# Kernel tuning notes

Measured on AMD Instinct MI355X. Metric: run time of the kernel, lower is better.

The kernel has to match this reference:

```python
import jax, jax.numpy as jnp
import numpy as np

V, E, H = 1024, 32, 64
D = 8                     # number of tree levels (root at depth 0)
PER = 149796              # nodes per non-root level
N = 1 + 7 * PER           # 1048573 total nodes


def setup_inputs() -> dict:
    rng = np.random.default_rng(0)
    sizes = [1] + [PER] * (D - 1)
    off = np.concatenate([[0], np.cumsum(sizes)])
    depth = np.repeat(np.arange(D), sizes).astype(np.int64)
    parent = np.zeros(N, dtype=np.int64)  # root points to itself (harmless: its h is 0 when read)
    for l in range(1, D):
        parent[off[l]:off[l + 1]] = rng.integers(off[l - 1], off[l], sizes[l])
    token_ids = rng.integers(0, V, N).astype(np.int64)

    key = jax.random.key(0)
    ks = jax.random.split(key, 7)
    s = 0.05
    return {
        "token_ids": jnp.asarray(token_ids),
        "parent": jnp.asarray(parent),
        "depth": jnp.asarray(depth),
        "max_depth": D - 1,
        "emb": jax.random.normal(ks[0], (V, E), jnp.float32) * s,
        "W_iou_w": jax.random.normal(ks[1], (3 * H, E), jnp.float32) * s,
        "W_iou_b": jax.random.normal(ks[2], (3 * H,), jnp.float32) * s,
        "U_iou_w": jax.random.normal(ks[3], (3 * H, H), jnp.float32) * s,
        "W_f_w": jax.random.normal(ks[4], (H, E), jnp.float32) * s,
        "W_f_b": jax.random.normal(ks[5], (H,), jnp.float32) * s,
        "U_f_w": jax.random.normal(ks[6], (H, H), jnp.float32) * s,
    }


def reference(token_ids, parent, depth, max_depth, emb,
              W_iou_w, W_iou_b, U_iou_w, W_f_w, W_f_b, U_f_w):
    n = token_ids.shape[0]
    hid = U_f_w.shape[0]
    x = emb[token_ids]                                 # [N, E]
    wiou_x = x @ W_iou_w.T + W_iou_b                   # [N, 3H] (input part, precomputed)
    wf_x = x @ W_f_w.T + W_f_b                         # [N, H]
    h = jnp.zeros((n, hid), x.dtype)
    c = jnp.zeros((n, hid), x.dtype)
    # level-synchronous bottom-up sweep (deepest level first); children of a
    # depth-d node are exactly at depth d+1, already finalized when d is processed
    for d in range(max_depth, -1, -1):
        h_sum = jax.ops.segment_sum(h, parent, num_segments=n)        # child-sum per parent
        f = jax.nn.sigmoid(wf_x[parent] + h @ U_f_w.T)                # forget gate per child edge
        fc = jax.ops.segment_sum(f * c, parent, num_segments=n)      # sum_k f_k * c_k per parent
        iou = wiou_x + h_sum @ U_iou_w.T
        i, o, u = jnp.split(iou, 3, axis=-1)
        c_new = jax.nn.sigmoid(i) * jnp.tanh(u) + fc
        h_new = jax.nn.sigmoid(o) * jnp.tanh(c_new)
        m = (depth == d)[:, None]
        h = jnp.where(m, h_new, h)
        c = jnp.where(m, c_new, c)
    return h[0]  # root hidden state, matching TreeLSTMEncoder.forward
```

## Files before the change

kernel.cpp:

```cpp
#include <hip/hip_runtime.h>
#include <hip/hip_fp16.h>
#include <string.h>

#define PER  149796
#define NN   1048573
#define HDIM 64
#define EDIM 32
#define NIOU 192

typedef _Float16 f16;
typedef _Float16 f16x8 __attribute__((ext_vector_type(8)));
typedef _Float16 f16x2 __attribute__((ext_vector_type(2)));
typedef float    f32x4 __attribute__((ext_vector_type(4)));

__device__ __forceinline__ float sigf(float x){ return 1.0f/(1.0f+__expf(-x)); }
__device__ __forceinline__ float tanh_f(float x){
  float ax = fabsf(x);
  float e  = __expf(-2.0f*ax);
  float t  = (1.0f - e)/(1.0f + e);
  return x < 0.0f ? -t : t;
}

__device__ __forceinline__ void atomAddH2(f16x2* p, f16 a, f16 b){
#if defined(__HIP_DEVICE_COMPILE__)
  typedef _Float16 h2 __attribute__((ext_vector_type(2)));
  h2 v; v[0]=a; v[1]=b;
  (void)__builtin_amdgcn_global_atomic_fadd_v2f16(
      (__attribute__((address_space(1))) h2*)p, v);
#else
  (void)p; (void)a; (void)b;
#endif
}

__global__ __launch_bounds__(256) void tablepack_kernel(
    const float* __restrict__ emb, const float* __restrict__ Wiou, const float* __restrict__ biou,
    const float* __restrict__ Wf, const float* __restrict__ bf,
    const float* __restrict__ Uf, const float* __restrict__ Uiou,
    float* __restrict__ embWiou, float* __restrict__ embWf,
    f16* __restrict__ Bfp, f16* __restrict__ Biop)
{
  if (blockIdx.x < 1024){
    int v = blockIdx.x;
    int m = threadIdx.x;
    const float* x = emb + (size_t)v*EDIM;
    if (m < NIOU){
      float a = biou[m];
      #pragma unroll
      for (int e=0;e<EDIM;e++) a += Wiou[m*EDIM+e]*x[e];
      embWiou[(size_t)v*NIOU + m] = a;
    } else {
      int mm = m - NIOU;
      float a = bf[mm];
      #pragma unroll
      for (int e=0;e<EDIM;e++) a += Wf[mm*EDIM+e]*x[e];
      embWf[(size_t)v*HDIM + mm] = a;
    }
  } else {
    for (int i = threadIdx.x; i < 2*4*64*8; i += 256){
      int j = i & 7, L = (i>>3)&63, st = i>>9;
      int t = st & 3, s = st >> 2;
      int k = s*32 + (L>>4)*8 + j;
      int n = t*16 + (L&15);
      Bfp[i] = (f16)Uf[n*HDIM + k];
    }
    for (int i = threadIdx.x; i < 2*12*64*8; i += 256){
      int j = i & 7, L = (i>>3)&63, st = i>>9;
      int t = st % 12, s = st / 12;
      int k = s*32 + (L>>4)*8 + j;
      int n = t*16 + (L&15);
      Biop[i] = (f16)Uiou[n*HDIM + k];
    }
  }
}

__global__ __launch_bounds__(64,4) void level_kernel(
    const int* __restrict__ tok, const int* __restrict__ parent,
    const float* __restrict__ embWiou, const float* __restrict__ embWf,
    const f16* __restrict__ Biopack, const f16* __restrict__ Ufpack,
    const f16x2* __restrict__ accIn, f16x2* __restrict__ accOut,
    int poff, int ppoff, int mode)
{
  __shared__ f16 Ah[16*72];
  __shared__ f16 FAf[16*68];
  int lane = threadIdx.x;
  int j0   = blockIdx.x*16;
  int q = lane>>4, c16 = lane&15;

  if (mode != 0){
    #pragma unroll
    for (int i=0;i<16;i++){
      int j = j0 + i; if (j > PER-1) j = PER-1;
      f16x2 v = accIn[(size_t)j*HDIM + lane];
      Ah[i*72 + lane]  = v.x;
      FAf[i*68 + lane] = v.y;
    }
  } else {
    #pragma unroll
    for (int i=0;i<16;i++){
      Ah[i*72 + lane]  = (f16)0.f;
      FAf[i*68 + lane] = (f16)0.f;
    }
  }
  __syncthreads();
  f16x8 A0 = *(const f16x8*)(Ah + c16*72 + q*8);
  f16x8 A1 = *(const f16x8*)(Ah + c16*72 + 32 + q*8);

  const f16x8* Bp = (const f16x8*)Biopack;
  f32x4 acc[12];
  #pragma unroll
  for (int nt=0;nt<12;nt++) acc[nt] = (f32x4){0.f,0.f,0.f,0.f};
  #pragma unroll
  for (int nt=0;nt<12;nt++){
    f16x8 B0 = Bp[nt*64 + lane];
    f16x8 B1 = Bp[(12+nt)*64 + lane];
    acc[nt] = __builtin_amdgcn_mfma_f32_16x16x32_f16(A0, B0, acc[nt], 0,0,0);
    acc[nt] = __builtin_amdgcn_mfma_f32_16x16x32_f16(A1, B1, acc[nt], 0,0,0);
  }
  float cc[4][4];
  f16   hh[4][4];
  int   prow_[4]; int wt_[4]; bool ok_[4];
  #pragma unroll
  for (int r=0;r<4;r++){
    int j = j0 + q*4 + r;
    bool ok = j < PER;
    int jl = ok ? j : PER-1;
    int g = poff + jl;
    int tk = tok[g];
    const float* tr = embWiou + (size_t)tk*NIOU;
    ok_[r] = ok;
    if (mode != 2){
      int pg = parent[g];
      prow_[r] = pg - ppoff;
      wt_[r]   = tok[pg];
    } else {
      prow_[r] = jl;
      wt_[r]   = tok[0];
    }
    int prow = q*4 + r;
    #pragma unroll
    for (int nt=0;nt<4;nt++){
      int col = nt*16 + c16;
      float ai = acc[nt][r]   + tr[col];
      float ao = acc[nt+4][r] + tr[64+col];
      float au = acc[nt+8][r] + tr[128+col];
      float fav = (float)FAf[prow*68 + col];
      float c = sigf(ai)*tanh_f(au) + fav;
      float h = sigf(ao)*tanh_f(c);
      cc[r][nt] = c;
      hh[r][nt] = (f16)h;
    }
  }
  __syncthreads();
  #pragma unroll
  for (int r=0;r<4;r++)
    #pragma unroll
    for (int nt=0;nt<4;nt++)
      Ah[(q*4+r)*72 + nt*16 + c16] = hh[r][nt];
  __syncthreads();
  f16x8 H0 = *(const f16x8*)(Ah + c16*72 + q*8);
  f16x8 H1 = *(const f16x8*)(Ah + c16*72 + 32 + q*8);
  const f16x8* Up = (const f16x8*)Ufpack;
  f32x4 g4[4];
  #pragma unroll
  for (int nt=0;nt<4;nt++) g4[nt] = (f32x4){0.f,0.f,0.f,0.f};
  #pragma unroll
  for (int nt=0;nt<4;nt++){
    f16x8 B0 = Up[nt*64 + lane];
    f16x8 B1 = Up[(4+nt)*64 + lane];
    g4[nt] = __builtin_amdgcn_mfma_f32_16x16x32_f16(H0, B0, g4[nt], 0,0,0);
    g4[nt] = __builtin_amdgcn_mfma_f32_16x16x32_f16(H1, B1, g4[nt], 0,0,0);
  }
  #pragma unroll
  for (int r=0;r<4;r++){
    if (!ok_[r]) continue;
    const float* wr = embWf + (size_t)wt_[r]*HDIM;
    size_t rb = (size_t)prow_[r]*HDIM;
    #pragma unroll
    for (int nt=0;nt<4;nt++){
      int col = nt*16 + c16;
      float v = sigf(g4[nt][r] + wr[col]) * cc[r][nt];
      if (mode == 2){
        f16x2 o; o.x = hh[r][nt]; o.y = (f16)v;
        accOut[rb + col] = o;
      } else {
        atomAddH2(&accOut[rb + col], hh[r][nt], (f16)v);
      }
    }
  }
}

__global__ __launch_bounds__(256) void rootred_kernel(
    const f16x2* __restrict__ HFin, float* __restrict__ rootacc)
{
  int t = blockIdx.x*blockDim.x + threadIdx.x;
  int m = t & 63;
  int j0 = t >> 6;
  int jstep = (gridDim.x*blockDim.x) >> 6;
  float af=0.f, ah=0.f;
  for (int j=j0; j<PER; j+=jstep){
    f16x2 v = HFin[(size_t)j*HDIM + m];
    ah += (float)v.x;
    af += (float)v.y;
  }
  __shared__ float red[256];
  red[threadIdx.x]=af; __syncthreads();
  if (threadIdx.x < 64) atomicAdd(&rootacc[m],    red[m]+red[64+m]+red[128+m]+red[192+m]);
  __syncthreads();
  red[threadIdx.x]=ah; __syncthreads();
  if (threadIdx.x < 64) atomicAdd(&rootacc[64+m], red[m]+red[64+m]+red[128+m]+red[192+m]);
}

__global__ void rootnode_kernel(
    const int* __restrict__ tok, const float* __restrict__ emb,
    const float* __restrict__ Wiou, const float* __restrict__ biou, const float* __restrict__ Uiou,
    const float* __restrict__ rootacc, float* __restrict__ out)
{
  int m = threadIdx.x;
  if (m >= HDIM) return;
  int t = tok[0];
  float ai=biou[m], ao=biou[HDIM+m], au=biou[2*HDIM+m];
  for (int e=0;e<EDIM;e++){
    float xe = emb[(size_t)t*EDIM+e];
    ai += Wiou[(size_t)m*EDIM+e]*xe;
    ao += Wiou[(size_t)(HDIM+m)*EDIM+e]*xe;
    au += Wiou[(size_t)(2*HDIM+m)*EDIM+e]*xe;
  }
  for (int k=0;k<HDIM;k++){
    float hv = rootacc[64+k];
    ai += Uiou[(size_t)m*HDIM+k]*hv;
    ao += Uiou[(size_t)(HDIM+m)*HDIM+k]*hv;
    au += Uiou[(size_t)(2*HDIM+m)*HDIM+k]*hv;
  }
  float c = sigf(ai)*tanh_f(au) + rootacc[m];
  out[m] = sigf(ao)*tanh_f(c);
}

static inline char* alignup(char* p){
  uintptr_t u = (uintptr_t)p;
  u = (u + 255) & ~(uintptr_t)255;
  return (char*)u;
}

extern "C" void kernel_launch(void* const* d_in, const int* in_sizes, int n_in,
                              void* d_out, int out_size, void* d_ws, size_t ws_size,
                              hipStream_t stream)
{
  const int*   tok    = (const int*)d_in[0];
  const int*   parent = (const int*)d_in[1];
  const float* emb    = (const float*)d_in[4];
  const float* Wiou   = (const float*)d_in[5];
  const float* biou   = (const float*)d_in[6];
  const float* Uiou   = (const float*)d_in[7];
  const float* Wf     = (const float*)d_in[8];
  const float* bf     = (const float*)d_in[9];
  const float* Uf     = (const float*)d_in[10];
  float* out = (float*)d_out;

  char* w = (char*)d_ws;
  size_t BUF = (size_t)PER*HDIM*sizeof(f16x2);
  f16x2* bufA    = (f16x2*)w;  w = alignup(w + BUF);
  f16x2* bufB    = (f16x2*)w;  w = alignup(w + BUF);
  float* embWiou = (float*)w;  w = alignup(w + 1024*NIOU*sizeof(float));
  float* embWf   = (float*)w;  w = alignup(w + 1024*HDIM*sizeof(float));
  float* rootacc = (float*)w;  w = alignup(w + 128*sizeof(float));
  f16*   Ufpack  = (f16*)w;    w = alignup(w + 2*4*64*8*sizeof(f16));
  f16*   Biopack = (f16*)w;    w = alignup(w + 2*12*64*8*sizeof(f16));

  const int NB = (PER + 15)/16;

  (void)hipMemsetAsync(rootacc, 0, 128*sizeof(float), stream);
  tablepack_kernel<<<1025, 256, 0, stream>>>(emb, Wiou, biou, Wf, bf, Uf, Uiou,
                                             embWiou, embWf, Ufpack, Biopack);

  f16x2* accIn  = nullptr;
  f16x2* accOut = bufA;
  (void)hipMemsetAsync(bufA, 0, BUF, stream);
  level_kernel<<<NB, 64, 0, stream>>>(tok, parent, embWiou, embWf, Biopack, Ufpack,
                                      nullptr, bufA, 1 + 6*PER, 1 + 5*PER, 0);
  accIn = bufA; accOut = bufB;
  for (int d=6; d>=2; --d){
    (void)hipMemsetAsync(accOut, 0, BUF, stream);
    level_kernel<<<NB, 64, 0, stream>>>(tok, parent, embWiou, embWf, Biopack, Ufpack,
                                        accIn, accOut, 1 + (d-1)*PER, 1 + (d-2)*PER, 1);
    f16x2* t2 = accIn; accIn = accOut; accOut = t2;
  }
  level_kernel<<<NB, 64, 0, stream>>>(tok, parent, embWiou, embWf, Biopack, Ufpack,
                                      accIn, accOut, 1, 0, 2);

  rootred_kernel<<<256, 256, 0, stream>>>(accOut, rootacc);
  rootnode_kernel<<<1, 64, 0, stream>>>(tok, emb, Wiou, biou, Uiou, rootacc, out);
}
```

Measured before the change: 550.6 us.

## Fuse input projections into level MFMA and zero consumed buffers in-kernel

Drops the precomputed per-token fp32 embWiou/embWf tables. The level kernel now gathers fp16 embeddings and runs the W_iou and W_f projections as an extra K=32 MFMA slice, adding the biases directly. Each block now holds four waves (256 threads) with per-wave shared tiles and no block barriers, and the leaf level skips the zero h-sum MFMAs. The per-level memsets are replaced by zeroing accIn inside the kernel after it is read. This trades large fp32 table gathers and memset launches for extra MFMA work and a reduced-precision input projection.

```diff
diff --git a/kernel.cpp b/kernel.cpp
--- a/kernel.cpp
+++ b/kernel.cpp
@@ -33,77 +33,83 @@
 }
 
 __global__ __launch_bounds__(256) void tablepack_kernel(
-    const float* __restrict__ emb, const float* __restrict__ Wiou, const float* __restrict__ biou,
-    const float* __restrict__ Wf, const float* __restrict__ bf,
+    const float* __restrict__ emb, const float* __restrict__ Wiou,
+    const float* __restrict__ Wf,
     const float* __restrict__ Uf, const float* __restrict__ Uiou,
-    float* __restrict__ embWiou, float* __restrict__ embWf,
+    f16* __restrict__ emb16,
     f16* __restrict__ Bfp, f16* __restrict__ Biop)
 {
   if (blockIdx.x < 1024){
     int v = blockIdx.x;
     int m = threadIdx.x;
-    const float* x = emb + (size_t)v*EDIM;
-    if (m < NIOU){
-      float a = biou[m];
-      #pragma unroll
-      for (int e=0;e<EDIM;e++) a += Wiou[m*EDIM+e]*x[e];
-      embWiou[(size_t)v*NIOU + m] = a;
-    } else {
-      int mm = m - NIOU;
-      float a = bf[mm];
-      #pragma unroll
-      for (int e=0;e<EDIM;e++) a += Wf[mm*EDIM+e]*x[e];
-      embWf[(size_t)v*HDIM + mm] = a;
-    }
+    if (m < EDIM) emb16[(size_t)v*EDIM + m] = (f16)emb[(size_t)v*EDIM + m];
   } else {
-    for (int i = threadIdx.x; i < 2*4*64*8; i += 256){
+    for (int i = threadIdx.x; i < 3*4*64*8; i += 256){
       int j = i & 7, L = (i>>3)&63, st = i>>9;
       int t = st & 3, s = st >> 2;
-      int k = s*32 + (L>>4)*8 + j;
+      int kk = (L>>4)*8 + j;
       int n = t*16 + (L&15);
-      Bfp[i] = (f16)Uf[n*HDIM + k];
-    }
-    for (int i = threadIdx.x; i < 2*12*64*8; i += 256){
+      Bfp[i] = (s < 2) ? (f16)Uf[n*HDIM + s*32 + kk]
+                       : (f16)Wf[n*EDIM + kk];
+    }
+    for (int i = threadIdx.x; i < 3*12*64*8; i += 256){
       int j = i & 7, L = (i>>3)&63, st = i>>9;
       int t = st % 12, s = st / 12;
-      int k = s*32 + (L>>4)*8 + j;
+      int kk = (L>>4)*8 + j;
       int n = t*16 + (L&15);
-      Biop[i] = (f16)Uiou[n*HDIM + k];
-    }
-  }
-}
-
-__global__ __launch_bounds__(64,4) void level_kernel(
+      Biop[i] = (s < 2) ? (f16)Uiou[n*HDIM + s*32 + kk]
+                        : (f16)Wiou[n*EDIM + kk];
+    }
+  }
+}
+
+__global__ __launch_bounds__(256,7) void level_kernel(
     const int* __restrict__ tok, const int* __restrict__ parent,
-    const float* __restrict__ embWiou, const float* __restrict__ embWf,
+    const f16* __restrict__ emb16,
+    const float* __restrict__ biou, const float* __restrict__ bf,
     const f16* __restrict__ Biopack, const f16* __restrict__ Ufpack,
     const f16x2* __restrict__ accIn, f16x2* __restrict__ accOut,
-    int poff, int ppoff, int mode)
-{
-  __shared__ f16 Ah[16*72];
-  __shared__ f16 FAf[16*68];
-  int lane = threadIdx.x;
-  int j0   = blockIdx.x*16;
+    int poff, int ppoff, int mode, int zin)
+{
+  __shared__ f16 Ah[4][16*104];
+  __shared__ f16 FAf[4][16*68];
+  int lane = threadIdx.x & 63;
+  int w    = threadIdx.x >> 6;
+  int j0   = (blockIdx.x*4 + w)*16;
   int q = lane>>4, c16 = lane&15;
-
+  f16* AhW  = &Ah[w][0];
+  f16* FAfW = &FAf[w][0];
+
+  {
+    int i  = lane>>2, cb = lane&3;
+    int j  = j0 + i; if (j > PER-1) j = PER-1;
+    int tk = tok[poff + j];
+    f16x8 xv = *(const f16x8*)(emb16 + (size_t)tk*EDIM + cb*8);
+    *(f16x8*)(AhW + i*104 + 64 + cb*8) = xv;
+  }
   if (mode != 0){
     #pragma unroll
     for (int i=0;i<16;i++){
       int j = j0 + i; if (j > PER-1) j = PER-1;
       f16x2 v = accIn[(size_t)j*HDIM + lane];
-      Ah[i*72 + lane]  = v.x;
-      FAf[i*68 + lane] = v.y;
+      AhW[i*104 + lane]  = v.x;
+      FAfW[i*68 + lane] = v.y;
     }
   } else {
     #pragma unroll
+    for (int i=0;i<16;i++)
+      FAfW[i*68 + lane] = (f16)0.f;
+  }
+  f16x8 A2 = *(const f16x8*)(AhW + c16*104 + 64 + q*8);
+
+  if (mode != 0 && zin){
+    f16x2 z; z.x = (f16)0.f; z.y = (f16)0.f;
+    #pragma unroll
     for (int i=0;i<16;i++){
-      Ah[i*72 + lane]  = (f16)0.f;
-      FAf[i*68 + lane] = (f16)0.f;
-    }
-  }
-  __syncthreads();
-  f16x8 A0 = *(const f16x8*)(Ah + c16*72 + q*8);
-  f16x8 A1 = *(const f16x8*)(Ah + c16*72 + 32 + q*8);
+      int j = j0 + i;
+      if (j < PER) ((f16x2*)accIn)[(size_t)j*HDIM + lane] = z;
+    }
+  }
 
   const f16x8* Bp = (const f16x8*)Biopack;
   f32x4 acc[12];
@@ -111,54 +117,61 @@
   for (int nt=0;nt<12;nt++) acc[nt] = (f32x4){0.f,0.f,0.f,0.f};
   #pragma unroll
   for (int nt=0;nt<12;nt++){
-    f16x8 B0 = Bp[nt*64 + lane];
-    f16x8 B1 = Bp[(12+nt)*64 + lane];
-    acc[nt] = __builtin_amdgcn_mfma_f32_16x16x32_f16(A0, B0, acc[nt], 0,0,0);
-    acc[nt] = __builtin_amdgcn_mfma_f32_16x16x32_f16(A1, B1, acc[nt], 0,0,0);
+    f16x8 B2 = Bp[(24+nt)*64 + lane];
+    acc[nt] = __builtin_amdgcn_mfma_f32_16x16x32_f16(A2, B2, acc[nt], 0,0,0);
+  }
+  if (mode != 0){
+    f16x8 A0 = *(const f16x8*)(AhW + c16*104 + q*8);
+    f16x8 A1 = *(const f16x8*)(AhW + c16*104 + 32 + q*8);
+    #pragma unroll
+    for (int nt=0;nt<12;nt++){
+      f16x8 B0 = Bp[nt*64 + lane];
+      f16x8 B1 = Bp[(12+nt)*64 + lane];
+      acc[nt] = __builtin_amdgcn_mfma_f32_16x16x32_f16(A0, B0, acc[nt], 0,0,0);
+      acc[nt] = __builtin_amdgcn_mfma_f32_16x16x32_f16(A1, B1, acc[nt], 0,0,0);
+    }
   }
   float cc[4][4];
   f16   hh[4][4];
-  int   prow_[4]; int wt_[4]; bool ok_[4];
+  int   prow_[4]; bool ok_[4];
   #pragma unroll
   for (int r=0;r<4;r++){
     int j = j0 + q*4 + r;
     bool ok = j < PER;
     int jl = ok ? j : PER-1;
     int g = poff + jl;
-    int tk = tok[g];
-    const float* tr = embWiou + (size_t)tk*NIOU;
     ok_[r] = ok;
-    if (mode != 2){
-      int pg = parent[g];
-      prow_[r] = pg - ppoff;
-      wt_[r]   = tok[pg];
-    } else {
-      prow_[r] = jl;
-      wt_[r]   = tok[0];
-    }
+    prow_[r] = (mode != 2) ? (parent[g] - ppoff) : jl;
     int prow = q*4 + r;
     #pragma unroll
     for (int nt=0;nt<4;nt++){
       int col = nt*16 + c16;
-      float ai = acc[nt][r]   + tr[col];
-      float ao = acc[nt+4][r] + tr[64+col];
-      float au = acc[nt+8][r] + tr[128+col];
-      float fav = (float)FAf[prow*68 + col];
+      float ai = acc[nt][r]   + biou[col];
+      float ao = acc[nt+4][r] + biou[64+col];
+      float au = acc[nt+8][r] + biou[128+col];
+      float fav = (float)FAfW[prow*68 + col];
       float c = sigf(ai)*tanh_f(au) + fav;
       float h = sigf(ao)*tanh_f(c);
       cc[r][nt] = c;
       hh[r][nt] = (f16)h;
     }
   }
-  __syncthreads();
   #pragma unroll
   for (int r=0;r<4;r++)
     #pragma unroll
     for (int nt=0;nt<4;nt++)
-      Ah[(q*4+r)*72 + nt*16 + c16] = hh[r][nt];
-  __syncthreads();
-  f16x8 H0 = *(const f16x8*)(Ah + c16*72 + q*8);
-  f16x8 H1 = *(const f16x8*)(Ah + c16*72 + 32 + q*8);
+      AhW[(q*4+r)*104 + nt*16 + c16] = hh[r][nt];
+  {
+    int i  = lane>>2, cb = lane&3;
+    int j  = j0 + i; if (j > PER-1) j = PER-1;
+    int pg = (mode != 2) ? parent[poff + j] : 0;
+    int ptk = tok[pg];
+    f16x8 pv = *(const f16x8*)(emb16 + (size_t)ptk*EDIM + cb*8);
+    *(f16x8*)(AhW + i*104 + 64 + cb*8) = pv;
+  }
+  f16x8 H0 = *(const f16x8*)(AhW + c16*104 + q*8);
+  f16x8 H1 = *(const f16x8*)(AhW + c16*104 + 32 + q*8);
+  f16x8 H2 = *(const f16x8*)(AhW + c16*104 + 64 + q*8);
   const f16x8* Up = (const f16x8*)Ufpack;
   f32x4 g4[4];
   #pragma unroll
@@ -167,18 +180,19 @@
   for (int nt=0;nt<4;nt++){
     f16x8 B0 = Up[nt*64 + lane];
     f16x8 B1 = Up[(4+nt)*64 + lane];
+    f16x8 B2 = Up[(8+nt)*64 + lane];
     g4[nt] = __builtin_amdgcn_mfma_f32_16x16x32_f16(H0, B0, g4[nt], 0,0,0);
     g4[nt] = __builtin_amdgcn_mfma_f32_16x16x32_f16(H1, B1, g4[nt], 0,0,0);
+    g4[nt] = __builtin_amdgcn_mfma_f32_16x16x32_f16(H2, B2, g4[nt], 0,0,0);
   }
   #pragma unroll
   for (int r=0;r<4;r++){
     if (!ok_[r]) continue;
-    const float* wr = embWf + (size_t)wt_[r]*HDIM;
     size_t rb = (size_t)prow_[r]*HDIM;
     #pragma unroll
     for (int nt=0;nt<4;nt++){
       int col = nt*16 + c16;
-      float v = sigf(g4[nt][r] + wr[col]) * cc[r][nt];
+      float v = sigf(g4[nt][r] + bf[col]) * cc[r][nt];
       if (mode == 2){
         f16x2 o; o.x = hh[r][nt]; o.y = (f16)v;
         accOut[rb + col] = o;
@@ -260,32 +274,32 @@
   size_t BUF = (size_t)PER*HDIM*sizeof(f16x2);
   f16x2* bufA    = (f16x2*)w;  w = alignup(w + BUF);
   f16x2* bufB    = (f16x2*)w;  w = alignup(w + BUF);
-  float* embWiou = (float*)w;  w = alignup(w + 1024*NIOU*sizeof(float));
-  float* embWf   = (float*)w;  w = alignup(w + 1024*HDIM*sizeof(float));
   float* rootacc = (float*)w;  w = alignup(w + 128*sizeof(float));
-  f16*   Ufpack  = (f16*)w;    w = alignup(w + 2*4*64*8*sizeof(f16));
-  f16*   Biopack = (f16*)w;    w = alignup(w + 2*12*64*8*sizeof(f16));
-
-  const int NB = (PER + 15)/16;
+  f16*   emb16   = (f16*)w;    w = alignup(w + 1024*EDIM*sizeof(f16));
+  f16*   Ufpack  = (f16*)w;    w = alignup(w + 3*4*64*8*sizeof(f16));
+  f16*   Biopack = (f16*)w;    w = alignup(w + 3*12*64*8*sizeof(f16));
+
+  const int NB = (PER + 63)/64;
 
   (void)hipMemsetAsync(rootacc, 0, 128*sizeof(float), stream);
-  tablepack_kernel<<<1025, 256, 0, stream>>>(emb, Wiou, biou, Wf, bf, Uf, Uiou,
-                                             embWiou, embWf, Ufpack, Biopack);
+  (void)hipMemsetAsync(bufA, 0, BUF, stream);
+  (void)hipMemsetAsync(bufB, 0, BUF, stream);
+  tablepack_kernel<<<1025, 256, 0, stream>>>(emb, Wiou, Wf, Uf, Uiou,
+                                             emb16, Ufpack, Biopack);
 
   f16x2* accIn  = nullptr;
   f16x2* accOut = bufA;
-  (void)hipMemsetAsync(bufA, 0, BUF, stream);
-  level_kernel<<<NB, 64, 0, stream>>>(tok, parent, embWiou, embWf, Biopack, Ufpack,
-                                      nullptr, bufA, 1 + 6*PER, 1 + 5*PER, 0);
+  level_kernel<<<NB, 256, 0, stream>>>(tok, parent, emb16, biou, bf, Biopack, Ufpack,
+                                       nullptr, bufA, 1 + 6*PER, 1 + 5*PER, 0, 0);
   accIn = bufA; accOut = bufB;
   for (int d=6; d>=2; --d){
-    (void)hipMemsetAsync(accOut, 0, BUF, stream);
-    level_kernel<<<NB, 64, 0, stream>>>(tok, parent, embWiou, embWf, Biopack, Ufpack,
-                                        accIn, accOut, 1 + (d-1)*PER, 1 + (d-2)*PER, 1);
+    level_kernel<<<NB, 256, 0, stream>>>(tok, parent, emb16, biou, bf, Biopack, Ufpack,
+                                         accIn, accOut, 1 + (d-1)*PER, 1 + (d-2)*PER, 1,
+                                         (d >= 3) ? 1 : 0);
     f16x2* t2 = accIn; accIn = accOut; accOut = t2;
   }
-  level_kernel<<<NB, 64, 0, stream>>>(tok, parent, embWiou, embWf, Biopack, Ufpack,
-                                      accIn, accOut, 1, 0, 2);
+  level_kernel<<<NB, 256, 0, stream>>>(tok, parent, emb16, biou, bf, Biopack, Ufpack,
+                                       accIn, accOut, 1, 0, 2, 0);
 
   rootred_kernel<<<256, 256, 0, stream>>>(accOut, rootacc);
   rootnode_kernel<<<1, 64, 0, stream>>>(tok, emb, Wiou, biou, Uiou, rootacc, out);
```

Measured after the change: 937.1 us. 1.7x slower.

## Pack IOU table as float4, use 4-wave blocks, fold buffer zeroing into kernel

Applied to the files above, without the earlier changes.

Repacks the per-token input-gate table so i/o/u for a column are fetched with one 16-byte load. Launches four 16-row tiles per 256-thread block with per-wave shared buffers instead of single-wave blocks. Replaces per-level hipMemsetAsync of the accumulation buffer with in-kernel zeroing of the consumed input buffer after it is read, removing separate memset passes. The in-kernel zeroing depends on buffer ping-pong parity, which risks leaving stale data in the final level's output buffer.

```diff
diff --git a/kernel.cpp b/kernel.cpp
--- a/kernel.cpp
+++ b/kernel.cpp
@@ -36,23 +36,29 @@
     const float* __restrict__ emb, const float* __restrict__ Wiou, const float* __restrict__ biou,
     const float* __restrict__ Wf, const float* __restrict__ bf,
     const float* __restrict__ Uf, const float* __restrict__ Uiou,
-    float* __restrict__ embWiou, float* __restrict__ embWf,
+    f32x4* __restrict__ packIOU, float* __restrict__ embWf,
     f16* __restrict__ Bfp, f16* __restrict__ Biop)
 {
   if (blockIdx.x < 1024){
     int v = blockIdx.x;
     int m = threadIdx.x;
     const float* x = emb + (size_t)v*EDIM;
-    if (m < NIOU){
-      float a = biou[m];
+    if (m < HDIM){
+      float a = biou[m], b = biou[HDIM+m], c = biou[2*HDIM+m];
       #pragma unroll
-      for (int e=0;e<EDIM;e++) a += Wiou[m*EDIM+e]*x[e];
-      embWiou[(size_t)v*NIOU + m] = a;
-    } else {
-      int mm = m - NIOU;
+      for (int e=0;e<EDIM;e++){
+        float xe = x[e];
+        a += Wiou[(size_t)m*EDIM+e]*xe;
+        b += Wiou[(size_t)(HDIM+m)*EDIM+e]*xe;
+        c += Wiou[(size_t)(2*HDIM+m)*EDIM+e]*xe;
+      }
+      f32x4 o; o.x=a; o.y=b; o.z=c; o.w=0.f;
+      packIOU[(size_t)v*HDIM + m] = o;
+    } else if (m < 2*HDIM){
+      int mm = m - HDIM;
       float a = bf[mm];
       #pragma unroll
-      for (int e=0;e<EDIM;e++) a += Wf[mm*EDIM+e]*x[e];
+      for (int e=0;e<EDIM;e++) a += Wf[(size_t)mm*EDIM+e]*x[e];
       embWf[(size_t)v*HDIM + mm] = a;
     }
   } else {
@@ -73,37 +79,49 @@
   }
 }
 
-__global__ __launch_bounds__(64,4) void level_kernel(
+__global__ __launch_bounds__(256,8) void level_kernel(
     const int* __restrict__ tok, const int* __restrict__ parent,
-    const float* __restrict__ embWiou, const float* __restrict__ embWf,
+    const f32x4* __restrict__ packIOU, const float* __restrict__ embWf,
     const f16* __restrict__ Biopack, const f16* __restrict__ Ufpack,
     const f16x2* __restrict__ accIn, f16x2* __restrict__ accOut,
-    int poff, int ppoff, int mode)
-{
-  __shared__ f16 Ah[16*72];
-  __shared__ f16 FAf[16*68];
-  int lane = threadIdx.x;
-  int j0   = blockIdx.x*16;
+    int poff, int ppoff, int mode, int zin)
+{
+  __shared__ f16 Ah[4][16*72];
+  __shared__ f16 FAf[4][16*68];
+  int lane = threadIdx.x & 63;
+  int w    = threadIdx.x >> 6;
+  int j0   = (blockIdx.x*4 + w)*16;
   int q = lane>>4, c16 = lane&15;
+  f16* AhW  = &Ah[w][0];
+  f16* FAfW = &FAf[w][0];
 
   if (mode != 0){
     #pragma unroll
     for (int i=0;i<16;i++){
       int j = j0 + i; if (j > PER-1) j = PER-1;
       f16x2 v = accIn[(size_t)j*HDIM + lane];
-      Ah[i*72 + lane]  = v.x;
-      FAf[i*68 + lane] = v.y;
+      AhW[i*72 + lane]  = v.x;
+      FAfW[i*68 + lane] = v.y;
     }
   } else {
     #pragma unroll
     for (int i=0;i<16;i++){
-      Ah[i*72 + lane]  = (f16)0.f;
-      FAf[i*68 + lane] = (f16)0.f;
+      AhW[i*72 + lane]  = (f16)0.f;
+      FAfW[i*68 + lane] = (f16)0.f;
     }
   }
   __syncthreads();
-  f16x8 A0 = *(const f16x8*)(Ah + c16*72 + q*8);
-  f16x8 A1 = *(const f16x8*)(Ah + c16*72 + 32 + q*8);
+  f16x8 A0 = *(const f16x8*)(AhW + c16*72 + q*8);
+  f16x8 A1 = *(const f16x8*)(AhW + c16*72 + 32 + q*8);
+
+  if (mode != 0 && zin){
+    f16x2 z; z.x = (f16)0.f; z.y = (f16)0.f;
+    #pragma unroll
+    for (int i=0;i<16;i++){
+      int j = j0 + i;
+      if (j < PER) ((f16x2*)accIn)[(size_t)j*HDIM + lane] = z;
+    }
+  }
 
   const f16x8* Bp = (const f16x8*)Biopack;
   f32x4 acc[12];
@@ -126,7 +144,7 @@
     int jl = ok ? j : PER-1;
     int g = poff + jl;
     int tk = tok[g];
-    const float* tr = embWiou + (size_t)tk*NIOU;
+    const f32x4* tr = packIOU + (size_t)tk*HDIM;
     ok_[r] = ok;
     if (mode != 2){
       int pg = parent[g];
@@ -140,10 +158,11 @@
     #pragma unroll
     for (int nt=0;nt<4;nt++){
       int col = nt*16 + c16;
-      float ai = acc[nt][r]   + tr[col];
-      float ao = acc[nt+4][r] + tr[64+col];
-      float au = acc[nt+8][r] + tr[128+col];
-      float fav = (float)FAf[prow*68 + col];
+      f32x4 wx = tr[col];
+      float ai = acc[nt][r]   + wx.x;
+      float ao = acc[nt+4][r] + wx.y;
+      float au = acc[nt+8][r] + wx.z;
+      float fav = (float)FAfW[prow*68 + col];
       float c = sigf(ai)*tanh_f(au) + fav;
       float h = sigf(ao)*tanh_f(c);
       cc[r][nt] = c;
@@ -155,10 +174,10 @@
   for (int r=0;r<4;r++)
     #pragma unroll
     for (int nt=0;nt<4;nt++)
-      Ah[(q*4+r)*72 + nt*16 + c16] = hh[r][nt];
+      AhW[(q*4+r)*72 + nt*16 + c16] = hh[r][nt];
   __syncthreads();
-  f16x8 H0 = *(const f16x8*)(Ah + c16*72 + q*8);
-  f16x8 H1 = *(const f16x8*)(Ah + c16*72 + 32 + q*8);
+  f16x8 H0 = *(const f16x8*)(AhW + c16*72 + q*8);
+  f16x8 H1 = *(const f16x8*)(AhW + c16*72 + 32 + q*8);
   const f16x8* Up = (const f16x8*)Ufpack;
   f32x4 g4[4];
   #pragma unroll
@@ -260,32 +279,33 @@
   size_t BUF = (size_t)PER*HDIM*sizeof(f16x2);
   f16x2* bufA    = (f16x2*)w;  w = alignup(w + BUF);
   f16x2* bufB    = (f16x2*)w;  w = alignup(w + BUF);
-  float* embWiou = (float*)w;  w = alignup(w + 1024*NIOU*sizeof(float));
+  f32x4* packIOU = (f32x4*)w;  w = alignup(w + (size_t)1024*HDIM*sizeof(f32x4));
   float* embWf   = (float*)w;  w = alignup(w + 1024*HDIM*sizeof(float));
   float* rootacc = (float*)w;  w = alignup(w + 128*sizeof(float));
   f16*   Ufpack  = (f16*)w;    w = alignup(w + 2*4*64*8*sizeof(f16));
   f16*   Biopack = (f16*)w;    w = alignup(w + 2*12*64*8*sizeof(f16));
 
-  const int NB = (PER + 15)/16;
+  const int NB = (PER + 63)/64;
 
   (void)hipMemsetAsync(rootacc, 0, 128*sizeof(float), stream);
+  (void)hipMemsetAsync(bufA, 0, BUF, stream);
+  (void)hipMemsetAsync(bufB, 0, BUF, stream);
   tablepack_kernel<<<1025, 256, 0, stream>>>(emb, Wiou, biou, Wf, bf, Uf, Uiou,
-                                             embWiou, embWf, Ufpack, Biopack);
+                                             packIOU, embWf, Ufpack, Biopack);
 
   f16x2* accIn  = nullptr;
   f16x2* accOut = bufA;
-  (void)hipMemsetAsync(bufA, 0, BUF, stream);
-  level_kernel<<<NB, 64, 0, stream>>>(tok, parent, embWiou, embWf, Biopack, Ufpack,
-                                      nullptr, bufA, 1 + 6*PER, 1 + 5*PER, 0);
+  level_kernel<<<NB, 256, 0, stream>>>(tok, parent, packIOU, embWf, Biopack, Ufpack,
+                                       nullptr, bufA, 1 + 6*PER, 1 + 5*PER, 0, 0);
   accIn = bufA; accOut = bufB;
   for (int d=6; d>=2; --d){
-    (void)hipMemsetAsync(accOut, 0, BUF, stream);
-    level_kernel<<<NB, 64, 0, stream>>>(tok, parent, embWiou, embWf, Biopack, Ufpack,
-                                        accIn, accOut, 1 + (d-1)*PER, 1 + (d-2)*PER, 1);
+    level_kernel<<<NB, 256, 0, stream>>>(tok, parent, packIOU, embWf, Biopack, Ufpack,
+                                         accIn, accOut, 1 + (d-1)*PER, 1 + (d-2)*PER, 1,
+                                         (d >= 3) ? 1 : 0);
     f16x2* t2 = accIn; accIn = accOut; accOut = t2;
   }
-  level_kernel<<<NB, 64, 0, stream>>>(tok, parent, embWiou, embWf, Biopack, Ufpack,
-                                      accIn, accOut, 1, 0, 2);
+  level_kernel<<<NB, 256, 0, stream>>>(tok, parent, packIOU, embWf, Biopack, Ufpack,
+                                       accIn, accOut, 1, 0, 2, 0);
 
   rootred_kernel<<<256, 256, 0, stream>>>(accOut, rootacc);
   rootnode_kernel<<<1, 64, 0, stream>>>(tok, emb, Wiou, biou, Uiou, rootacc, out);
```

Result: slower. 1.174 ms (+113.3%).
